# Performance work log

Measured on AMD Instinct MI355X. Metric: run time of the kernel, lower is better.

Reference implementation:

```python
import jax, jax.numpy as jnp
import numpy as np

B, S, D, H = 2, 2048, 1024, 16
HD = D // H  # head_dim = 64
EPS = 1e-12


def setup_inputs() -> dict:
    key = jax.random.key(0)
    ks = jax.random.split(key, 12)
    s = 0.02
    return {
        "hidden_states": jax.random.normal(ks[0], (B, S, D), jnp.float32),
        "attention_mask": jnp.zeros((B, 1, 1, S), jnp.float32),
        "alibi_bias": jax.random.normal(ks[1], (1, H, S, S), jnp.float32) * 0.1,
        "Wq": jax.random.normal(ks[2], (D, D), jnp.float32) * s,
        "bq": jnp.zeros((D,), jnp.float32),
        "Wk": jax.random.normal(ks[3], (D, D), jnp.float32) * s,
        "bk": jnp.zeros((D,), jnp.float32),
        "Wv": jax.random.normal(ks[4], (D, D), jnp.float32) * s,
        "bv": jnp.zeros((D,), jnp.float32),
        "Wo": jax.random.normal(ks[5], (D, D), jnp.float32) * s,
        "bo": jnp.zeros((D,), jnp.float32),
        "ln_gamma": jnp.ones((D,), jnp.float32),
        "ln_beta": jnp.zeros((D,), jnp.float32),
    }


def _split_heads(x):
    # [B, S, D] -> [B, H, S, HD]
    return x.reshape(B, S, H, HD).transpose(0, 2, 1, 3)


def reference(hidden_states, attention_mask, alibi_bias,
              Wq, bq, Wk, bk, Wv, bv, Wo, bo, ln_gamma, ln_beta):
    q = _split_heads(hidden_states @ Wq + bq)
    k = _split_heads(hidden_states @ Wk + bk)
    v = _split_heads(hidden_states @ Wv + bv)

    scale = HD ** -0.5
    # combined additive mask: [B,1,1,S] + [1,H,S,S] -> broadcast [B,H,S,S]
    combined_mask = attention_mask + alibi_bias
    scores = jnp.einsum('bhqd,bhkd->bhqk', q, k) * scale + combined_mask
    probs = jax.nn.softmax(scores, axis=-1)
    attn = jnp.einsum('bhqk,bhkd->bhqd', probs, v)  # [B,H,S,HD]
    attn = attn.transpose(0, 2, 1, 3).reshape(B, S, D)

    out = attn @ Wo + bo
    x = hidden_states + out  # post-norm residual
    mu = jnp.mean(x, axis=-1, keepdims=True)
    var = jnp.mean(jnp.square(x - mu), axis=-1, keepdims=True)
    return (x - mu) * jax.lax.rsqrt(var + EPS) * ln_gamma + ln_beta
```

## Files before the change

### kernel.cpp

```cpp
#include <hip/hip_runtime.h>

#define Bb 2
#define Ss 2048
#define Dd 1024
#define Hh 16
#define HD 64
#define Mm (Bb*Ss)

typedef __bf16 bf16;
typedef __bf16 bf16x8 __attribute__((ext_vector_type(8)));
typedef float f32x4 __attribute__((ext_vector_type(4)));

__global__ void cvt_f32_bf16(const float* __restrict__ in, bf16* __restrict__ out, int n4) {
    int i = blockIdx.x * blockDim.x + threadIdx.x;
    if (i < n4) {
        float4 v = *(const float4*)(in + i * 4);
        out[i*4+0] = (bf16)v.x; out[i*4+1] = (bf16)v.y;
        out[i*4+2] = (bf16)v.z; out[i*4+3] = (bf16)v.w;
    }
}

__global__ void wtrans(const float* __restrict__ W0, const float* __restrict__ W1,
                       const float* __restrict__ W2, const float* __restrict__ W3,
                       bf16* __restrict__ O0, bf16* __restrict__ O1,
                       bf16* __restrict__ O2, bf16* __restrict__ O3) {
    const float* W = (blockIdx.z == 0) ? W0 : (blockIdx.z == 1) ? W1 : (blockIdx.z == 2) ? W2 : W3;
    bf16* O = (blockIdx.z == 0) ? O0 : (blockIdx.z == 1) ? O1 : (blockIdx.z == 2) ? O2 : O3;
    __shared__ bf16 t[64][65];
    int k0 = blockIdx.x * 64, n0 = blockIdx.y * 64;
    for (int c = threadIdx.x; c < 4096; c += 256) {
        int r = c >> 6, cc = c & 63;
        t[r][cc] = (bf16)W[(k0 + r) * Dd + n0 + cc];
    }
    __syncthreads();
    for (int c = threadIdx.x; c < 4096; c += 256) {
        int r = c >> 6, cc = c & 63;
        O[(n0 + r) * Dd + k0 + cc] = t[cc][r];
    }
}

__global__ __launch_bounds__(256, 2)
void gemm_bt(const bf16* __restrict__ A, const bf16* __restrict__ Bt,
             const float* __restrict__ bias, bf16* __restrict__ out, int mode) {
    const int K = 1024, N = 1024;
    __shared__ __align__(16) bf16 As[128 * 32];
    __shared__ __align__(16) bf16 Bs[128 * 32];
    int tid = threadIdx.x;
    int wave = tid >> 6, lane = tid & 63;
    int lane15 = lane & 15, quad = lane >> 4;
    int wm = (wave >> 1) * 64, wn = (wave & 1) * 64;
    int m0 = blockIdx.x * 128, n0 = blockIdx.y * 128;
    int srow = tid >> 2;
    int skoff = (tid & 3) * 8;

    f32x4 acc[4][4] = {};

    for (int kt = 0; kt < K; kt += 32) {
        __syncthreads();
        *(bf16x8*)(&As[srow * 32 + skoff])        = *(const bf16x8*)(&A[(m0 + srow) * K + kt + skoff]);
        *(bf16x8*)(&As[(srow + 64) * 32 + skoff]) = *(const bf16x8*)(&A[(m0 + srow + 64) * K + kt + skoff]);
        *(bf16x8*)(&Bs[srow * 32 + skoff])        = *(const bf16x8*)(&Bt[(n0 + srow) * K + kt + skoff]);
        *(bf16x8*)(&Bs[(srow + 64) * 32 + skoff]) = *(const bf16x8*)(&Bt[(n0 + srow + 64) * K + kt + skoff]);
        __syncthreads();
        bf16x8 af[4], bfr[4];
#pragma unroll
        for (int i = 0; i < 4; i++) af[i] = *(const bf16x8*)(&As[(wm + i * 16 + lane15) * 32 + quad * 8]);
#pragma unroll
        for (int j = 0; j < 4; j++) bfr[j] = *(const bf16x8*)(&Bs[(wn + j * 16 + lane15) * 32 + quad * 8]);
#pragma unroll
        for (int i = 0; i < 4; i++)
#pragma unroll
            for (int j = 0; j < 4; j++)
                acc[i][j] = __builtin_amdgcn_mfma_f32_16x16x32_bf16(af[i], bfr[j], acc[i][j], 0, 0, 0);
    }

#pragma unroll
    for (int i = 0; i < 4; i++) {
        int mbase = m0 + wm + i * 16 + quad * 4;
#pragma unroll
        for (int j = 0; j < 4; j++) {
            int n = n0 + wn + j * 16 + lane15;
            float bv = bias[n];
#pragma unroll
            for (int r = 0; r < 4; r++) {
                float v = acc[i][j][r] + bv;
                int m = mbase + r;
                if (mode == 0) {
                    out[m * N + n] = (bf16)v;
                } else {
                    int b = m >> 11, s = m & 2047, h = n >> 6, hd = n & 63;
                    out[(((size_t)(b * Hh + h) * Ss + s) * HD) + hd] = (bf16)v;
                }
            }
        }
    }
}

__global__ __launch_bounds__(256, 2)
void attn_kernel(const bf16* __restrict__ Q, const bf16* __restrict__ Kk, const bf16* __restrict__ V,
                 const float* __restrict__ alibi, const float* __restrict__ mask,
                 bf16* __restrict__ outattn) {
    int qt = blockIdx.x, h = blockIdx.y, b = blockIdx.z;
    __shared__ __align__(16) bf16 Qs[64 * 64];
    __shared__ __align__(16) bf16 Ks[64 * 64];
    __shared__ __align__(16) bf16 Vts[64 * 64];
    __shared__ __align__(16) bf16 Ps[64 * 64];
    int tid = threadIdx.x, wave = tid >> 6, lane = tid & 63;
    int lane15 = lane & 15, quad = lane >> 4;

    const bf16* Qbase = Q + ((size_t)(b * Hh + h) * Ss + qt * 64) * HD;
    const bf16* Kbase = Kk + (size_t)(b * Hh + h) * Ss * HD;
    const bf16* Vbase = V + (size_t)(b * Hh + h) * Ss * HD;

    for (int c = tid; c < 512; c += 256) {
        int r = c >> 3, off = (c & 7) * 8;
        *(bf16x8*)(&Qs[r * 64 + off]) = *(const bf16x8*)(&Qbase[r * HD + off]);
    }
    __syncthreads();
    bf16x8 qf0 = *(const bf16x8*)(&Qs[(wave * 16 + lane15) * 64 + quad * 8]);
    bf16x8 qf1 = *(const bf16x8*)(&Qs[(wave * 16 + lane15) * 64 + 32 + quad * 8]);

    float m_i[4], l_i[4];
    f32x4 O[4] = {};
#pragma unroll
    for (int r = 0; r < 4; r++) { m_i[r] = -1e30f; l_i[r] = 0.f; }

    const float scale = 0.125f;
    const float* alibi_base = alibi + ((size_t)h * Ss + qt * 64 + wave * 16 + quad * 4) * Ss;
    const float* mask_base = mask + b * Ss;

    for (int kt = 0; kt < Ss; kt += 64) {
        __syncthreads();
        for (int c = tid; c < 512; c += 256) {
            int r = c >> 3, off = (c & 7) * 8;
            *(bf16x8*)(&Ks[r * 64 + off]) = *(const bf16x8*)(&Kbase[(kt + r) * HD + off]);
        }
        for (int c = tid; c < 512; c += 256) {
            int r = c >> 3, off = (c & 7) * 8;
            bf16x8 v = *(const bf16x8*)(&Vbase[(kt + r) * HD + off]);
#pragma unroll
            for (int e = 0; e < 8; e++) Vts[(off + e) * 64 + r] = v[e];
        }
        __syncthreads();

        f32x4 sc[4];
        f32x4 z = {0.f, 0.f, 0.f, 0.f};
#pragma unroll
        for (int j = 0; j < 4; j++) {
            bf16x8 kf0 = *(const bf16x8*)(&Ks[(j * 16 + lane15) * 64 + quad * 8]);
            bf16x8 kf1 = *(const bf16x8*)(&Ks[(j * 16 + lane15) * 64 + 32 + quad * 8]);
            f32x4 s = __builtin_amdgcn_mfma_f32_16x16x32_bf16(qf0, kf0, z, 0, 0, 0);
            s = __builtin_amdgcn_mfma_f32_16x16x32_bf16(qf1, kf1, s, 0, 0, 0);
            sc[j] = s;
        }
#pragma unroll
        for (int j = 0; j < 4; j++) {
            int col = kt + j * 16 + lane15;
            float mk = mask_base[col];
#pragma unroll
            for (int r = 0; r < 4; r++) {
                float al = alibi_base[(size_t)r * Ss + col];
                sc[j][r] = sc[j][r] * scale + al + mk;
            }
        }
        float alpha[4];
#pragma unroll
        for (int r = 0; r < 4; r++) {
            float v = fmaxf(fmaxf(sc[0][r], sc[1][r]), fmaxf(sc[2][r], sc[3][r]));
#pragma unroll
            for (int d = 1; d < 16; d <<= 1) v = fmaxf(v, __shfl_xor(v, d, 64));
            float mnew = fmaxf(m_i[r], v);
            alpha[r] = __expf(m_i[r] - mnew);
            m_i[r] = mnew;
        }
        float rs[4] = {0.f, 0.f, 0.f, 0.f};
#pragma unroll
        for (int j = 0; j < 4; j++)
#pragma unroll
            for (int r = 0; r < 4; r++) {
                float p = __expf(sc[j][r] - m_i[r]);
                sc[j][r] = p;
                rs[r] += p;
            }
#pragma unroll
        for (int r = 0; r < 4; r++) {
            float v = rs[r];
#pragma unroll
            for (int d = 1; d < 16; d <<= 1) v += __shfl_xor(v, d, 64);
            l_i[r] = l_i[r] * alpha[r] + v;
        }
#pragma unroll
        for (int j = 0; j < 4; j++)
#pragma unroll
            for (int r = 0; r < 4; r++)
                Ps[(wave * 16 + quad * 4 + r) * 64 + j * 16 + lane15] = (bf16)sc[j][r];
        __syncthreads();

        bf16x8 pf0 = *(const bf16x8*)(&Ps[(wave * 16 + lane15) * 64 + quad * 8]);
        bf16x8 pf1 = *(const bf16x8*)(&Ps[(wave * 16 + lane15) * 64 + 32 + quad * 8]);
#pragma unroll
        for (int jd = 0; jd < 4; jd++) {
#pragma unroll
            for (int r = 0; r < 4; r++) O[jd][r] *= alpha[r];
            bf16x8 vf0 = *(const bf16x8*)(&Vts[(jd * 16 + lane15) * 64 + quad * 8]);
            bf16x8 vf1 = *(const bf16x8*)(&Vts[(jd * 16 + lane15) * 64 + 32 + quad * 8]);
            O[jd] = __builtin_amdgcn_mfma_f32_16x16x32_bf16(pf0, vf0, O[jd], 0, 0, 0);
            O[jd] = __builtin_amdgcn_mfma_f32_16x16x32_bf16(pf1, vf1, O[jd], 0, 0, 0);
        }
    }

#pragma unroll
    for (int jd = 0; jd < 4; jd++) {
        int d = jd * 16 + lane15;
#pragma unroll
        for (int r = 0; r < 4; r++) {
            int qg = qt * 64 + wave * 16 + quad * 4 + r;
            float v = O[jd][r] / l_i[r];
            outattn[(((size_t)b * Ss + qg) * Hh + h) * HD + d] = (bf16)v;
        }
    }
}

__global__ void ln_kernel(const float* __restrict__ hidden, const bf16* __restrict__ Y,
                          const float* __restrict__ gamma, const float* __restrict__ beta,
                          float* __restrict__ out) {
    int row = blockIdx.x;
    int tid = threadIdx.x, wave = tid >> 6, lane = tid & 63;
    float x[4];
    float s = 0.f, q = 0.f;
#pragma unroll
    for (int e = 0; e < 4; e++) {
        int col = e * 256 + tid;
        x[e] = hidden[(size_t)row * Dd + col] + (float)Y[(size_t)row * Dd + col];
        s += x[e];
        q += x[e] * x[e];
    }
#pragma unroll
    for (int d = 1; d < 64; d <<= 1) { s += __shfl_xor(s, d, 64); q += __shfl_xor(q, d, 64); }
    __shared__ float sm[4], sq[4];
    if (lane == 0) { sm[wave] = s; sq[wave] = q; }
    __syncthreads();
    float tot = sm[0] + sm[1] + sm[2] + sm[3];
    float totq = sq[0] + sq[1] + sq[2] + sq[3];
    float mu = tot * (1.f / 1024.f);
    float var = totq * (1.f / 1024.f) - mu * mu;
    float rstd = rsqrtf(var + 1e-12f);
#pragma unroll
    for (int e = 0; e < 4; e++) {
        int col = e * 256 + tid;
        out[(size_t)row * Dd + col] = (x[e] - mu) * rstd * gamma[col] + beta[col];
    }
}

extern "C" void kernel_launch(void* const* d_in, const int* in_sizes, int n_in,
                              void* d_out, int out_size, void* d_ws, size_t ws_size,
                              hipStream_t stream) {
    const float* hidden = (const float*)d_in[0];
    const float* amask  = (const float*)d_in[1];
    const float* alibi  = (const float*)d_in[2];
    const float* Wq = (const float*)d_in[3];
    const float* bq = (const float*)d_in[4];
    const float* Wk = (const float*)d_in[5];
    const float* bk = (const float*)d_in[6];
    const float* Wv = (const float*)d_in[7];
    const float* bv = (const float*)d_in[8];
    const float* Wo = (const float*)d_in[9];
    const float* bo = (const float*)d_in[10];
    const float* ln_g = (const float*)d_in[11];
    const float* ln_b = (const float*)d_in[12];
    float* out = (float*)d_out;

    char* w = (char*)d_ws;
    bf16* Xb   = (bf16*)(w);
    bf16* WqT  = (bf16*)(w + 8388608);
    bf16* WkT  = (bf16*)(w + 10485760);
    bf16* WvT  = (bf16*)(w + 12582912);
    bf16* WoT  = (bf16*)(w + 14680064);
    bf16* Qw   = (bf16*)(w + 16777216);
    bf16* Kw   = (bf16*)(w + 25165824);
    bf16* Vw   = (bf16*)(w + 33554432);
    bf16* Attn = (bf16*)(w + 41943040);
    bf16* Yw   = (bf16*)(w + 50331648);

    cvt_f32_bf16<<<4096, 256, 0, stream>>>(hidden, Xb, Mm * Dd / 4);
    wtrans<<<dim3(16, 16, 4), 256, 0, stream>>>(Wq, Wk, Wv, Wo, WqT, WkT, WvT, WoT);

    gemm_bt<<<dim3(32, 8), 256, 0, stream>>>(Xb, WqT, bq, Qw, 1);
    gemm_bt<<<dim3(32, 8), 256, 0, stream>>>(Xb, WkT, bk, Kw, 1);
    gemm_bt<<<dim3(32, 8), 256, 0, stream>>>(Xb, WvT, bv, Vw, 1);

    attn_kernel<<<dim3(32, 16, 2), 256, 0, stream>>>(Qw, Kw, Vw, alibi, amask, Attn);

    gemm_bt<<<dim3(32, 8), 256, 0, stream>>>(Attn, WoT, bo, Yw, 0);

    ln_kernel<<<4096, 256, 0, stream>>>(hidden, Yw, ln_g, ln_b, out);
}
```

Before: 647.8 us.

## Fuse QKV GEMMs, use direct-to-LDS loads, and restructure attention without shared K/V

The three Q/K/V projections become one GEMM launch over a concatenated N=3072, relying on WqT/WkT/WvT being contiguous in the workspace. That GEMM folds the softmax scale into Q, and all GEMM tile loads now go global-to-LDS directly. A separate kernel pre-transposes V. The attention kernel drops shared K/V tiles and block-wide barriers: each wave reads K and V^T straight from global memory, starts the QK MFMA accumulator from the alibi+mask values, and swaps P through a small per-wave LDS buffer. The output GEMM uses 128x64 tiles for more blocks. Trade-offs are repeated global K/V reads across waves and an extra V transpose pass.

```diff
diff --git a/kernel.cpp b/kernel.cpp
--- a/kernel.cpp
+++ b/kernel.cpp
@@ -9,7 +9,13 @@
 
 typedef __bf16 bf16;
 typedef __bf16 bf16x8 __attribute__((ext_vector_type(8)));
+typedef __bf16 bf16x4 __attribute__((ext_vector_type(4)));
 typedef float f32x4 __attribute__((ext_vector_type(4)));
+
+__device__ __forceinline__ void gl2lds(const bf16* g, bf16* l) {
+    __builtin_amdgcn_global_load_lds((const __attribute__((address_space(1))) unsigned int*)g,
+                                     (__attribute__((address_space(3))) unsigned int*)l, 16, 0, 0);
+}
 
 __global__ void cvt_f32_bf16(const float* __restrict__ in, bf16* __restrict__ out, int n4) {
     int i = blockIdx.x * blockDim.x + threadIdx.x;
@@ -39,129 +45,146 @@
     }
 }
 
+__global__ void bcat(const float* __restrict__ bq, const float* __restrict__ bk,
+                     const float* __restrict__ bv, float* __restrict__ o) {
+    int i = blockIdx.x * 256 + threadIdx.x;
+    const float* s = (i < 1024) ? bq : (i < 2048) ? bk : bv;
+    o[i] = s[i & 1023];
+}
+
+__global__ void vtrans(const bf16* __restrict__ Vw, bf16* __restrict__ Vt) {
+    int st = blockIdx.x, h = blockIdx.y, b = blockIdx.z;
+    __shared__ bf16 t[64][65];
+    const bf16* src = Vw + ((size_t)(b * Hh + h) * Ss + st * 64) * HD;
+    bf16* dst = Vt + (size_t)(b * Hh + h) * HD * Ss + st * 64;
+    for (int c = threadIdx.x; c < 4096; c += 256) {
+        int r = c >> 6, cc = c & 63;
+        t[r][cc] = src[r * HD + cc];
+    }
+    __syncthreads();
+    for (int c = threadIdx.x; c < 4096; c += 256) {
+        int r = c >> 6, cc = c & 63;
+        dst[(size_t)r * Ss + cc] = t[cc][r];
+    }
+}
+
+template<int BN, int MODE>
 __global__ __launch_bounds__(256, 2)
-void gemm_bt(const bf16* __restrict__ A, const bf16* __restrict__ Bt,
-             const float* __restrict__ bias, bf16* __restrict__ out, int mode) {
-    const int K = 1024, N = 1024;
+void gemm2(const bf16* __restrict__ A, const bf16* __restrict__ Bt,
+           const float* __restrict__ bias, bf16* __restrict__ outp) {
+    const int K = 1024;
     __shared__ __align__(16) bf16 As[128 * 32];
-    __shared__ __align__(16) bf16 Bs[128 * 32];
-    int tid = threadIdx.x;
-    int wave = tid >> 6, lane = tid & 63;
+    __shared__ __align__(16) bf16 Bs[BN * 32];
+    int tid = threadIdx.x, wave = tid >> 6, lane = tid & 63;
     int lane15 = lane & 15, quad = lane >> 4;
-    int wm = (wave >> 1) * 64, wn = (wave & 1) * 64;
-    int m0 = blockIdx.x * 128, n0 = blockIdx.y * 128;
-    int srow = tid >> 2;
-    int skoff = (tid & 3) * 8;
-
-    f32x4 acc[4][4] = {};
+    int m0 = blockIdx.x * 128, n0 = blockIdx.y * BN;
+    int sr = lane >> 2, sc8 = (lane & 3) * 8;
+
+    const bf16* Aga = A + (size_t)(m0 + wave * 32 + sr) * K + sc8;
+    const bf16* Agb = Aga + (size_t)16 * K;
+    bf16* lA0 = As + (wave * 32) * 32;
+    bf16* lA1 = As + (wave * 32 + 16) * 32;
+
+    const bf16* Bga; const bf16* Bgb = nullptr;
+    bf16* lB0; bf16* lB1 = nullptr;
+    if constexpr (BN == 128) {
+        Bga = Bt + (size_t)(n0 + wave * 32 + sr) * K + sc8;
+        Bgb = Bga + (size_t)16 * K;
+        lB0 = Bs + (wave * 32) * 32;
+        lB1 = Bs + (wave * 32 + 16) * 32;
+    } else {
+        Bga = Bt + (size_t)(n0 + wave * 16 + sr) * K + sc8;
+        lB0 = Bs + (wave * 16) * 32;
+    }
+
+    constexpr int NI = (BN == 128) ? 4 : 2;
+    const int WM = (BN == 128) ? ((wave >> 1) * 64) : (wave * 32);
+    const int WN = (BN == 128) ? ((wave & 1) * 64) : 0;
+
+    f32x4 acc[NI][4] = {};
 
     for (int kt = 0; kt < K; kt += 32) {
         __syncthreads();
-        *(bf16x8*)(&As[srow * 32 + skoff])        = *(const bf16x8*)(&A[(m0 + srow) * K + kt + skoff]);
-        *(bf16x8*)(&As[(srow + 64) * 32 + skoff]) = *(const bf16x8*)(&A[(m0 + srow + 64) * K + kt + skoff]);
-        *(bf16x8*)(&Bs[srow * 32 + skoff])        = *(const bf16x8*)(&Bt[(n0 + srow) * K + kt + skoff]);
-        *(bf16x8*)(&Bs[(srow + 64) * 32 + skoff]) = *(const bf16x8*)(&Bt[(n0 + srow + 64) * K + kt + skoff]);
+        gl2lds(Aga + kt, lA0);
+        gl2lds(Agb + kt, lA1);
+        gl2lds(Bga + kt, lB0);
+        if constexpr (BN == 128) gl2lds(Bgb + kt, lB1);
         __syncthreads();
-        bf16x8 af[4], bfr[4];
-#pragma unroll
-        for (int i = 0; i < 4; i++) af[i] = *(const bf16x8*)(&As[(wm + i * 16 + lane15) * 32 + quad * 8]);
-#pragma unroll
-        for (int j = 0; j < 4; j++) bfr[j] = *(const bf16x8*)(&Bs[(wn + j * 16 + lane15) * 32 + quad * 8]);
-#pragma unroll
-        for (int i = 0; i < 4; i++)
+        bf16x8 af[NI], bfr[4];
+#pragma unroll
+        for (int i = 0; i < NI; i++) af[i] = *(const bf16x8*)(&As[(WM + i * 16 + lane15) * 32 + quad * 8]);
+#pragma unroll
+        for (int j = 0; j < 4; j++) bfr[j] = *(const bf16x8*)(&Bs[(WN + j * 16 + lane15) * 32 + quad * 8]);
+#pragma unroll
+        for (int i = 0; i < NI; i++)
 #pragma unroll
             for (int j = 0; j < 4; j++)
                 acc[i][j] = __builtin_amdgcn_mfma_f32_16x16x32_bf16(af[i], bfr[j], acc[i][j], 0, 0, 0);
     }
 
 #pragma unroll
-    for (int i = 0; i < 4; i++) {
-        int mbase = m0 + wm + i * 16 + quad * 4;
+    for (int i = 0; i < NI; i++) {
+        int mbase = m0 + WM + i * 16 + quad * 4;
 #pragma unroll
         for (int j = 0; j < 4; j++) {
-            int n = n0 + wn + j * 16 + lane15;
+            int n = n0 + WN + j * 16 + lane15;
             float bv = bias[n];
 #pragma unroll
             for (int r = 0; r < 4; r++) {
                 float v = acc[i][j][r] + bv;
                 int m = mbase + r;
-                if (mode == 0) {
-                    out[m * N + n] = (bf16)v;
+                if constexpr (MODE == 0) {
+                    outp[(size_t)m * 1024 + n] = (bf16)v;
                 } else {
-                    int b = m >> 11, s = m & 2047, h = n >> 6, hd = n & 63;
-                    out[(((size_t)(b * Hh + h) * Ss + s) * HD) + hd] = (bf16)v;
+                    int b = m >> 11, s = m & 2047;
+                    int sel = n >> 10, h = (n >> 6) & 15, hd = n & 63;
+                    float scl = (sel == 0) ? 0.125f : 1.0f;
+                    outp[(size_t)sel * 4194304 +
+                         (((size_t)(b * Hh + h) * Ss + s) * HD) + hd] = (bf16)(v * scl);
                 }
             }
         }
     }
 }
 
-__global__ __launch_bounds__(256, 2)
-void attn_kernel(const bf16* __restrict__ Q, const bf16* __restrict__ Kk, const bf16* __restrict__ V,
-                 const float* __restrict__ alibi, const float* __restrict__ mask,
-                 bf16* __restrict__ outattn) {
+__global__ __launch_bounds__(256, 3)
+void attn2(const bf16* __restrict__ Q, const bf16* __restrict__ Kk, const bf16* __restrict__ Vt,
+           const float* __restrict__ alibi, const float* __restrict__ mask,
+           bf16* __restrict__ outa) {
     int qt = blockIdx.x, h = blockIdx.y, b = blockIdx.z;
-    __shared__ __align__(16) bf16 Qs[64 * 64];
-    __shared__ __align__(16) bf16 Ks[64 * 64];
-    __shared__ __align__(16) bf16 Vts[64 * 64];
-    __shared__ __align__(16) bf16 Ps[64 * 64];
     int tid = threadIdx.x, wave = tid >> 6, lane = tid & 63;
     int lane15 = lane & 15, quad = lane >> 4;
-
-    const bf16* Qbase = Q + ((size_t)(b * Hh + h) * Ss + qt * 64) * HD;
-    const bf16* Kbase = Kk + (size_t)(b * Hh + h) * Ss * HD;
-    const bf16* Vbase = V + (size_t)(b * Hh + h) * Ss * HD;
-
-    for (int c = tid; c < 512; c += 256) {
-        int r = c >> 3, off = (c & 7) * 8;
-        *(bf16x8*)(&Qs[r * 64 + off]) = *(const bf16x8*)(&Qbase[r * HD + off]);
-    }
-    __syncthreads();
-    bf16x8 qf0 = *(const bf16x8*)(&Qs[(wave * 16 + lane15) * 64 + quad * 8]);
-    bf16x8 qf1 = *(const bf16x8*)(&Qs[(wave * 16 + lane15) * 64 + 32 + quad * 8]);
-
-    float m_i[4], l_i[4];
+    __shared__ __align__(16) bf16 Pt[4][64 * 20];
+    bf16* Ptw = Pt[wave];
+
+    const bf16* Qb = Q + ((size_t)(b * Hh + h) * Ss + qt * 64 + wave * 16) * HD;
+    const bf16* Kb = Kk + (size_t)(b * Hh + h) * Ss * HD;
+    const bf16* Vb = Vt + (size_t)(b * Hh + h) * HD * Ss;
+    const float* ab = alibi + ((size_t)h * Ss + qt * 64 + wave * 16 + quad * 4) * Ss;
+    const float* mb = mask + (size_t)b * Ss;
+
+    bf16x8 qf0 = *(const bf16x8*)(Qb + lane15 * HD + quad * 8);
+    bf16x8 qf1 = *(const bf16x8*)(Qb + lane15 * HD + 32 + quad * 8);
+
+    float m_i[4] = {-1e30f, -1e30f, -1e30f, -1e30f}, l_i[4] = {0.f, 0.f, 0.f, 0.f};
     f32x4 O[4] = {};
-#pragma unroll
-    for (int r = 0; r < 4; r++) { m_i[r] = -1e30f; l_i[r] = 0.f; }
-
-    const float scale = 0.125f;
-    const float* alibi_base = alibi + ((size_t)h * Ss + qt * 64 + wave * 16 + quad * 4) * Ss;
-    const float* mask_base = mask + b * Ss;
 
     for (int kt = 0; kt < Ss; kt += 64) {
-        __syncthreads();
-        for (int c = tid; c < 512; c += 256) {
-            int r = c >> 3, off = (c & 7) * 8;
-            *(bf16x8*)(&Ks[r * 64 + off]) = *(const bf16x8*)(&Kbase[(kt + r) * HD + off]);
-        }
-        for (int c = tid; c < 512; c += 256) {
-            int r = c >> 3, off = (c & 7) * 8;
-            bf16x8 v = *(const bf16x8*)(&Vbase[(kt + r) * HD + off]);
-#pragma unroll
-            for (int e = 0; e < 8; e++) Vts[(off + e) * 64 + r] = v[e];
-        }
-        __syncthreads();
-
         f32x4 sc[4];
-        f32x4 z = {0.f, 0.f, 0.f, 0.f};
+        float mk[4];
+#pragma unroll
+        for (int j = 0; j < 4; j++) mk[j] = mb[kt + j * 16 + lane15];
 #pragma unroll
         for (int j = 0; j < 4; j++) {
-            bf16x8 kf0 = *(const bf16x8*)(&Ks[(j * 16 + lane15) * 64 + quad * 8]);
-            bf16x8 kf1 = *(const bf16x8*)(&Ks[(j * 16 + lane15) * 64 + 32 + quad * 8]);
-            f32x4 s = __builtin_amdgcn_mfma_f32_16x16x32_bf16(qf0, kf0, z, 0, 0, 0);
-            s = __builtin_amdgcn_mfma_f32_16x16x32_bf16(qf1, kf1, s, 0, 0, 0);
-            sc[j] = s;
-        }
-#pragma unroll
-        for (int j = 0; j < 4; j++) {
-            int col = kt + j * 16 + lane15;
-            float mk = mask_base[col];
-#pragma unroll
-            for (int r = 0; r < 4; r++) {
-                float al = alibi_base[(size_t)r * Ss + col];
-                sc[j][r] = sc[j][r] * scale + al + mk;
-            }
+            f32x4 ini;
+#pragma unroll
+            for (int r = 0; r < 4; r++)
+                ini[r] = __builtin_nontemporal_load(&ab[(size_t)r * Ss + kt + j * 16 + lane15]) + mk[j];
+            const bf16* kp = Kb + (size_t)(kt + j * 16 + lane15) * HD + quad * 8;
+            bf16x8 kf0 = *(const bf16x8*)(kp);
+            bf16x8 kf1 = *(const bf16x8*)(kp + 32);
+            sc[j] = __builtin_amdgcn_mfma_f32_16x16x32_bf16(qf0, kf0, ini, 0, 0, 0);
+            sc[j] = __builtin_amdgcn_mfma_f32_16x16x32_bf16(qf1, kf1, sc[j], 0, 0, 0);
         }
         float alpha[4];
 #pragma unroll
@@ -190,33 +213,36 @@
             l_i[r] = l_i[r] * alpha[r] + v;
         }
 #pragma unroll
-        for (int j = 0; j < 4; j++)
-#pragma unroll
-            for (int r = 0; r < 4; r++)
-                Ps[(wave * 16 + quad * 4 + r) * 64 + j * 16 + lane15] = (bf16)sc[j][r];
-        __syncthreads();
-
-        bf16x8 pf0 = *(const bf16x8*)(&Ps[(wave * 16 + lane15) * 64 + quad * 8]);
-        bf16x8 pf1 = *(const bf16x8*)(&Ps[(wave * 16 + lane15) * 64 + 32 + quad * 8]);
+        for (int j = 0; j < 4; j++) {
+            bf16x4 pw;
+#pragma unroll
+            for (int r = 0; r < 4; r++) pw[r] = (bf16)sc[j][r];
+            *(bf16x4*)(&Ptw[(j * 16 + lane15) * 20 + quad * 4]) = pw;
+        }
+        bf16x8 pf0, pf1;
+#pragma unroll
+        for (int jj = 0; jj < 8; jj++) {
+            pf0[jj] = Ptw[(quad * 8 + jj) * 20 + lane15];
+            pf1[jj] = Ptw[(32 + quad * 8 + jj) * 20 + lane15];
+        }
 #pragma unroll
         for (int jd = 0; jd < 4; jd++) {
 #pragma unroll
             for (int r = 0; r < 4; r++) O[jd][r] *= alpha[r];
-            bf16x8 vf0 = *(const bf16x8*)(&Vts[(jd * 16 + lane15) * 64 + quad * 8]);
-            bf16x8 vf1 = *(const bf16x8*)(&Vts[(jd * 16 + lane15) * 64 + 32 + quad * 8]);
+            const bf16* vp = Vb + (size_t)(jd * 16 + lane15) * Ss + kt + quad * 8;
+            bf16x8 vf0 = *(const bf16x8*)(vp);
+            bf16x8 vf1 = *(const bf16x8*)(vp + 32);
             O[jd] = __builtin_amdgcn_mfma_f32_16x16x32_bf16(pf0, vf0, O[jd], 0, 0, 0);
             O[jd] = __builtin_amdgcn_mfma_f32_16x16x32_bf16(pf1, vf1, O[jd], 0, 0, 0);
         }
     }
-
 #pragma unroll
     for (int jd = 0; jd < 4; jd++) {
         int d = jd * 16 + lane15;
 #pragma unroll
         for (int r = 0; r < 4; r++) {
             int qg = qt * 64 + wave * 16 + quad * 4 + r;
-            float v = O[jd][r] / l_i[r];
-            outattn[(((size_t)b * Ss + qg) * Hh + h) * HD + d] = (bf16)v;
+            outa[((size_t)b * Ss + qg) * Dd + h * HD + d] = (bf16)(O[jd][r] / l_i[r]);
         }
     }
 }
@@ -271,27 +297,29 @@
     float* out = (float*)d_out;
 
     char* w = (char*)d_ws;
-    bf16* Xb   = (bf16*)(w);
-    bf16* WqT  = (bf16*)(w + 8388608);
-    bf16* WkT  = (bf16*)(w + 10485760);
-    bf16* WvT  = (bf16*)(w + 12582912);
-    bf16* WoT  = (bf16*)(w + 14680064);
-    bf16* Qw   = (bf16*)(w + 16777216);
-    bf16* Kw   = (bf16*)(w + 25165824);
-    bf16* Vw   = (bf16*)(w + 33554432);
-    bf16* Attn = (bf16*)(w + 41943040);
-    bf16* Yw   = (bf16*)(w + 50331648);
+    bf16*  Xb    = (bf16*)(w);
+    bf16*  WqT   = (bf16*)(w + 8388608);
+    bf16*  WkT   = (bf16*)(w + 10485760);
+    bf16*  WvT   = (bf16*)(w + 12582912);
+    bf16*  WoT   = (bf16*)(w + 14680064);
+    float* bQKV  = (float*)(w + 16777216);
+    bf16*  Qw    = (bf16*)(w + 16793600);
+    bf16*  Vw    = (bf16*)(w + 16793600 + 2 * 8388608);
+    bf16*  Vtw   = (bf16*)(w + 41959424);
+    bf16*  Attn  = (bf16*)(w + 50348032);
+    bf16*  Yw    = (bf16*)(w + 58736640);
 
     cvt_f32_bf16<<<4096, 256, 0, stream>>>(hidden, Xb, Mm * Dd / 4);
     wtrans<<<dim3(16, 16, 4), 256, 0, stream>>>(Wq, Wk, Wv, Wo, WqT, WkT, WvT, WoT);
-
-    gemm_bt<<<dim3(32, 8), 256, 0, stream>>>(Xb, WqT, bq, Qw, 1);
-    gemm_bt<<<dim3(32, 8), 256, 0, stream>>>(Xb, WkT, bk, Kw, 1);
-    gemm_bt<<<dim3(32, 8), 256, 0, stream>>>(Xb, WvT, bv, Vw, 1);
-
-    attn_kernel<<<dim3(32, 16, 2), 256, 0, stream>>>(Qw, Kw, Vw, alibi, amask, Attn);
-
-    gemm_bt<<<dim3(32, 8), 256, 0, stream>>>(Attn, WoT, bo, Yw, 0);
+    bcat<<<12, 256, 0, stream>>>(bq, bk, bv, bQKV);
+
+    gemm2<128, 1><<<dim3(32, 24), 256, 0, stream>>>(Xb, WqT, bQKV, Qw);
+
+    vtrans<<<dim3(32, 16, 2), 256, 0, stream>>>(Vw, Vtw);
+
+    attn2<<<dim3(32, 16, 2), 256, 0, stream>>>(Qw, Qw + 4194304, Vtw, alibi, amask, Attn);
+
+    gemm2<64, 0><<<dim3(32, 16), 256, 0, stream>>>(Attn, WoT, bo, Yw);
 
     ln_kernel<<<4096, 256, 0, stream>>>(hidden, Yw, ln_g, ln_b, out);
 }
```

After: 685.5 us. 5.8% more time.
